# Kernel tuning notes

Measured on AMD Instinct MI355X. Metric: run time of the kernel, lower is better.

Reference implementation:

```python
import jax, jax.numpy as jnp
import numpy as np

WEIGHT_SP = 0.1
BANDWIDTH = 0.5
EPS = 1e-5


def _l2_normalize(v, axis, eps=1e-12):
    # matches torch F.normalize(p=2): x / max(||x||, eps)
    n = jnp.sqrt(jnp.sum(v * v, axis=axis, keepdims=True))
    return v / jnp.maximum(n, eps)


def _compute_meshgrid(N, H, W):
    rows = jnp.arange(H, dtype=jnp.float32) / (H + 1)
    cols = jnp.arange(W, dtype=jnp.float32) / (W + 1)
    gr, gc = jnp.meshgrid(rows, cols, indexing="ij")
    grid = jnp.stack([gr, gc])[None]  # (1, 2, H, W)
    return jnp.broadcast_to(grid, (N, 2, H, W))


def _l2_distance(x, y):
    # Faithful to the torch code; its broadcasting is only valid for N == 1.
    N, C, H, W = x.shape
    xv = x.reshape(N, C, -1)
    yv = y.reshape(N, C, -1)
    x_s = jnp.sum(xv ** 2, axis=1)          # (N, HW)
    y_s = jnp.sum(yv ** 2, axis=1)          # (N, HW)
    A = jnp.einsum("nci,ncj->nij", yv, xv)  # (N, HW, HW)
    dist = y_s - 2.0 * A + x_s.T            # same broadcast as torch (N==1)
    dist = jnp.swapaxes(dist, 1, 2)         # transpose(1,2); reshape is no-op
    return jnp.maximum(dist, 0.0)


def _cosine_distance(x, y):
    y_mu = jnp.mean(y, axis=(0, 2, 3), keepdims=True)   # (1, C, 1, 1)
    xn = _l2_normalize(x - y_mu, axis=1)
    yn = _l2_normalize(y - y_mu, axis=1)
    N, C = x.shape[:2]
    xn = xn.reshape(N, C, -1)
    yn = yn.reshape(N, C, -1)
    cos = jnp.einsum("nci,ncj->nij", xn, yn)            # (N, HW, HW)
    return 1.0 - cos


def _relative_distance(dist, eps=1e-5):
    dmin = jnp.min(dist, axis=2, keepdims=True)
    return dist / (dmin + eps)


def _compute_cx(dist_tilde, bandwidth):
    w = jnp.exp((1.0 - dist_tilde) / bandwidth)
    return w / jnp.sum(w, axis=2, keepdims=True)


def setup_inputs() -> dict:
    key = jax.random.key(0)
    k1, k2 = jax.random.split(key)
    x = jax.random.normal(k1, (1, 512, 80, 80), dtype=jnp.float32)
    y = jax.random.normal(k2, (1, 512, 80, 80), dtype=jnp.float32)
    return {"x": x, "y": y}


def reference(x, y):
    N, C, H, W = x.shape
    # spatial branch
    grid = _compute_meshgrid(N, H, W)
    cx_sp = _compute_cx(_relative_distance(_l2_distance(grid, grid), 1e-5), BANDWIDTH)
    # feature branch (loss_type == 'cosine')
    cx_feat = _compute_cx(_relative_distance(_cosine_distance(x, y), EPS), BANDWIDTH)
    cx_combine = (1.0 - WEIGHT_SP) * cx_feat + WEIGHT_SP * cx_sp
    k_max = jnp.max(cx_combine, axis=2, keepdims=True)  # (N, HW, 1)
    cx = jnp.mean(k_max, axis=1)                        # (N, 1)
    return jnp.mean(-jnp.log(cx + EPS))
```

## Files before the change

### kernel.cpp

```cpp
#include <hip/hip_runtime.h>
#include <hip/hip_bf16.h>
#include <math.h>

#define HW 6400
#define NC 512
#define NH 80
#define NW 80
#define NCH 25
#define NSLOT 50
#define NCYS 4
#define JCH 256
#define TI 128
#define BK 64
#define NT16 400
#define NCG 100

typedef __attribute__((ext_vector_type(8))) short short8;
typedef __attribute__((ext_vector_type(4))) float v4f;

#define MU_OFF    0
#define ACC_OFF   512
#define GMAXP_OFF (ACC_OFF + 64)
#define GDIAG_OFF (GMAXP_OFF + HW*NSLOT)
#define ZP_OFF    (GDIAG_OFF + HW)
#define F32_FLOATS (ZP_OFF + HW*NSLOT)
#define XB_BYTE   ((size_t)(((F32_FLOATS*4) + 255) & ~255))
#define YB_BYTE   (XB_BYTE + (size_t)HW*NC*2)
#define G_BYTE    (YB_BYTE + (size_t)HW*NC*2)
#define G_BYTES   ((size_t)NT16 * NT16 * 256)

typedef __attribute__((address_space(1))) unsigned int uint_g;
typedef __attribute__((address_space(3))) unsigned int uint_l;
__device__ __forceinline__ void gload16(const void* g, void* l) {
    __builtin_amdgcn_global_load_lds((const uint_g*)g, (uint_l*)l, 16, 0, 0);
}

__global__ void k_mu(const float* __restrict__ y, float* __restrict__ mu,
                     float* __restrict__ acczero) {
    if (blockIdx.x == 0 && threadIdx.x < 64) acczero[threadIdx.x] = 0.f;
    int c = blockIdx.x;
    const float4* yc4 = (const float4*)(y + (size_t)c * HW);
    float s = 0.f;
    for (int i = threadIdx.x; i < HW / 4; i += 256) {
        float4 v = yc4[i];
        s += (v.x + v.y) + (v.z + v.w);
    }
    __shared__ float red[256];
    red[threadIdx.x] = s;
    __syncthreads();
    for (int off = 128; off > 0; off >>= 1) {
        if (threadIdx.x < off) red[threadIdx.x] += red[threadIdx.x + off];
        __syncthreads();
    }
    if (threadIdx.x == 0) mu[c] = red[0] * (1.0f / HW);
}

__global__ void k_prep(const float* __restrict__ x, const float* __restrict__ y,
                       const float* __restrict__ mu,
                       unsigned short* __restrict__ xb, unsigned short* __restrict__ yb) {
    __shared__ float smu[NC];
    __shared__ float part[64][17];
    __shared__ float ssinv[64];
    __shared__ float tile[64 * 65];
    const int t = threadIdx.x;
    const int i0 = blockIdx.x * 64;
    const int z = blockIdx.y;
    const float* src = z ? y : x;
    unsigned short* dst = z ? yb : xb;

    for (int c = t; c < NC; c += 256) smu[c] = mu[c];
    __syncthreads();

    const int p0 = (t & 15) * 4;
    const int g  = t >> 4;
    float a0 = 0.f, a1 = 0.f, a2 = 0.f, a3 = 0.f;
    #pragma unroll 2
    for (int ch = 0; ch < 8; ++ch) {
        #pragma unroll
        for (int it = 0; it < 4; ++it) {
            int cl = ch * 64 + it * 16 + g;
            float m = smu[cl];
            float4 v = *(const float4*)(src + (size_t)cl * HW + i0 + p0);
            float d0 = v.x - m, d1 = v.y - m, d2 = v.z - m, d3 = v.w - m;
            a0 = fmaf(d0, d0, a0); a1 = fmaf(d1, d1, a1);
            a2 = fmaf(d2, d2, a2); a3 = fmaf(d3, d3, a3);
        }
    }
    part[p0 + 0][g] = a0; part[p0 + 1][g] = a1;
    part[p0 + 2][g] = a2; part[p0 + 3][g] = a3;
    __syncthreads();
    if (t < 64) {
        float s = 0.f;
        #pragma unroll
        for (int k = 0; k < 16; ++k) s += part[t][k];
        ssinv[t] = 1.0f / fmaxf(sqrtf(s), 1e-12f);
    }
    __syncthreads();

    for (int ch = 0; ch < 8; ++ch) {
        #pragma unroll
        for (int it = 0; it < 4; ++it) {
            int cl = ch * 64 + it * 16 + g;
            float m = smu[cl];
            float4 v = *(const float4*)(src + (size_t)cl * HW + i0 + p0);
            int clo = it * 16 + g;
            tile[(p0 + 0) * 65 + clo] = (v.x - m) * ssinv[p0 + 0];
            tile[(p0 + 1) * 65 + clo] = (v.y - m) * ssinv[p0 + 1];
            tile[(p0 + 2) * 65 + clo] = (v.z - m) * ssinv[p0 + 2];
            tile[(p0 + 3) * 65 + clo] = (v.w - m) * ssinv[p0 + 3];
        }
        __syncthreads();
        #pragma unroll
        for (int it = 0; it < 2; ++it) {
            int il = t >> 2;
            int seg = (t & 3) + it * 4;
            unsigned int pk[4];
            #pragma unroll
            for (int p = 0; p < 4; ++p) {
                float v0 = tile[il * 65 + seg * 8 + p * 2];
                float v1 = tile[il * 65 + seg * 8 + p * 2 + 1];
                __hip_bfloat16 h0 = __float2bfloat16(v0);
                __hip_bfloat16 h1 = __float2bfloat16(v1);
                unsigned short u0 = *reinterpret_cast<unsigned short*>(&h0);
                unsigned short u1 = *reinterpret_cast<unsigned short*>(&h1);
                pk[p] = (unsigned int)u0 | ((unsigned int)u1 << 16);
            }
            uint4 val = make_uint4(pk[0], pk[1], pk[2], pk[3]);
            *(uint4*)&dst[(size_t)(i0 + il) * NC + ch * 64 + seg * 8] = val;
        }
        __syncthreads();
    }
}

__device__ __forceinline__ void rmax_epilogue(float (&rmax)[16], float* gmaxp,
                                              int i0, int wr, int wc, int lr, int lg) {
    #pragma unroll
    for (int u = 0; u < 16; ++u) {
        float v = rmax[u];
        v = fmaxf(v, __shfl_xor(v, 1));
        v = fmaxf(v, __shfl_xor(v, 2));
        v = fmaxf(v, __shfl_xor(v, 4));
        v = fmaxf(v, __shfl_xor(v, 8));
        if (lr == 0) {
            int row = i0 + wr * 64 + (u >> 2) * 16 + lg * 4 + (u & 3);
            gmaxp[(size_t)row * NSLOT + blockIdx.y * 2 + wc] = v;
        }
    }
}

template <typename F>
__device__ __forceinline__ void gemm_driver(const unsigned short* __restrict__ Xb,
                                            const unsigned short* __restrict__ Yb,
                                            F&& consume) {
    __shared__ char sA[TI * BK * 2];
    __shared__ char sB[TI * BK * 2];
    const int t = threadIdx.x;
    const int w = t >> 6, l = t & 63;
    const int wr = w >> 1, wc = w & 1;
    const int lr = l & 15, lg = l >> 4;
    const int i0 = blockIdx.x * TI;
    const int jbase = blockIdx.y * JCH;

    int aoff[4][2], boff[4][2];
    #pragma unroll
    for (int mt = 0; mt < 4; ++mt) {
        int row = wr * 64 + mt * 16 + lr;
        #pragma unroll
        for (int ks = 0; ks < 2; ++ks) {
            int seg = ks * 4 + lg;
            aoff[mt][ks] = row * 128 + ((seg ^ (row & 7)) * 16);
        }
    }
    #pragma unroll
    for (int nt = 0; nt < 4; ++nt) {
        int row = wc * 64 + nt * 16 + lr;
        #pragma unroll
        for (int ks = 0; ks < 2; ++ks) {
            int seg = ks * 4 + lg;
            boff[nt][ks] = row * 128 + ((seg ^ (row & 7)) * 16);
        }
    }
    const int strow = l >> 3;
    const int stcol = ((l & 7) ^ strow) * 8;
    char* dA0 = sA + (w * 4 + 0) * 1024;
    char* dA1 = sA + (w * 4 + 1) * 1024;
    char* dA2 = sA + (w * 4 + 2) * 1024;
    char* dA3 = sA + (w * 4 + 3) * 1024;
    char* dB0 = sB + (w * 4 + 0) * 1024;
    char* dB1 = sB + (w * 4 + 1) * 1024;
    char* dB2 = sB + (w * 4 + 2) * 1024;
    char* dB3 = sB + (w * 4 + 3) * 1024;
    const unsigned short* ga = Xb + (size_t)(i0 + w * 32 + strow) * NC + stcol;
    const unsigned short* gb0 = Yb + (size_t)(jbase + w * 32 + strow) * NC + stcol;

    #pragma unroll 1
    for (int jt = 0; jt < JCH; jt += TI) {
        const unsigned short* gb = gb0 + (size_t)jt * NC;
        v4f acc[4][4];
        #pragma unroll
        for (int mt = 0; mt < 4; ++mt)
            #pragma unroll
            for (int nt = 0; nt < 4; ++nt)
                acc[mt][nt] = (v4f){0.f, 0.f, 0.f, 0.f};

        #pragma unroll 1
        for (int kt = 0; kt < NC; kt += BK) {
            __syncthreads();
            gload16(ga + kt,           dA0);
            gload16(ga + 8  * NC + kt, dA1);
            gload16(ga + 16 * NC + kt, dA2);
            gload16(ga + 24 * NC + kt, dA3);
            gload16(gb + kt,           dB0);
            gload16(gb + 8  * NC + kt, dB1);
            gload16(gb + 16 * NC + kt, dB2);
            gload16(gb + 24 * NC + kt, dB3);
            __syncthreads();
            #pragma unroll
            for (int ks = 0; ks < 2; ++ks) {
                short8 af[4], bf[4];
                #pragma unroll
                for (int mt = 0; mt < 4; ++mt) af[mt] = *(const short8*)&sA[aoff[mt][ks]];
                #pragma unroll
                for (int nt = 0; nt < 4; ++nt) bf[nt] = *(const short8*)&sB[boff[nt][ks]];
                #pragma unroll
                for (int mt = 0; mt < 4; ++mt)
                    #pragma unroll
                    for (int nt = 0; nt < 4; ++nt)
                        acc[mt][nt] = __builtin_amdgcn_mfma_f32_16x16x32_bf16(
                            af[mt], bf[nt], acc[mt][nt], 0, 0, 0);
            }
        }
        consume(acc, jt);
    }
}

__global__ __launch_bounds__(256, 2) void k_pass1s(const unsigned short* __restrict__ Xb,
                                                   const unsigned short* __restrict__ Yb,
                                                   float* __restrict__ gmaxp,
                                                   float* __restrict__ gdiag,
                                                   unsigned int* __restrict__ G1) {
    const int t = threadIdx.x;
    const int w = t >> 6, l = t & 63;
    const int wr = w >> 1, wc = w & 1;
    const int lr = l & 15, lg = l >> 4;
    const int i0 = blockIdx.x * TI;
    const int jbase = blockIdx.y * JCH;
    float rmax[16];
    #pragma unroll
    for (int u = 0; u < 16; ++u) rmax[u] = -3.0e38f;

    gemm_driver(Xb, Yb, [&](v4f (&acc)[4][4], int jt) {
        const bool diagblk = (jbase + jt == i0);
        const int cg = (jbase + jt) / 64 + wc;
        #pragma unroll
        for (int mt = 0; mt < 4; ++mt) {
            unsigned int pks[4];
            #pragma unroll
            for (int nt = 0; nt < 4; ++nt) {
                float g0 = acc[mt][nt][0];
                float g1 = acc[mt][nt][1];
                float g2 = acc[mt][nt][2];
                float g3 = acc[mt][nt][3];
                rmax[mt * 4 + 0] = fmaxf(rmax[mt * 4 + 0], g0);
                rmax[mt * 4 + 1] = fmaxf(rmax[mt * 4 + 1], g1);
                rmax[mt * 4 + 2] = fmaxf(rmax[mt * 4 + 2], g2);
                rmax[mt * 4 + 3] = fmaxf(rmax[mt * 4 + 3], g3);
                unsigned int pk = __builtin_amdgcn_cvt_pk_fp8_f32(g0, g1, 0, false);
                pk = __builtin_amdgcn_cvt_pk_fp8_f32(g2, g3, pk, true);
                pks[nt] = pk;
                if (diagblk) {
                    int rowb = i0 + wr * 64 + mt * 16 + lg * 4;
                    int col = jbase + jt + wc * 64 + nt * 16 + lr;
                    if (col == rowb + 0) gdiag[col] = g0;
                    if (col == rowb + 1) gdiag[col] = g1;
                    if (col == rowb + 2) gdiag[col] = g2;
                    if (col == rowb + 3) gdiag[col] = g3;
                }
            }
            size_t idx = ((size_t)(i0 / 16 + wr * 4 + mt) * NCG + cg) * 64 + l;
            ((uint4*)G1)[idx] = make_uint4(pks[0], pks[1], pks[2], pks[3]);
        }
    });
    rmax_epilogue(rmax, gmaxp, i0, wr, wc, lr, lg);
}

__global__ __launch_bounds__(256) void k_pass2s(const unsigned int* __restrict__ G1,
                                                const float* __restrict__ gmaxp,
                                                float* __restrict__ zp) {
    const int t = threadIdx.x;
    const int w = t >> 6, l = t & 63;
    const int lr = l & 15, lg = l >> 4;
    const int rt = blockIdx.x * 4 + w;
    const int cy = blockIdx.y;

    float m = -3.0e38f;
    {
        int row = rt * 16 + lr;
        #pragma unroll
        for (int k = 0; k < 13; ++k) {
            int s = lg + 4 * k;
            if (s < NSLOT) m = fmaxf(m, gmaxp[(size_t)row * NSLOT + s]);
        }
        m = fmaxf(m, __shfl_xor(m, 16));
        m = fmaxf(m, __shfl_xor(m, 32));
    }
    float inv_lr = 1.0f / ((1.0f - m) + 1e-5f);
    float c1[4], c2[4];
    #pragma unroll
    for (int r = 0; r < 4; ++r) {
        float iv = __shfl(inv_lr, lg * 4 + r);
        c2[r] = 2.0f * iv;
        c1[r] = 2.0f - 2.0f * iv;
    }

    const uint4* base = (const uint4*)G1 + (size_t)rt * (NCG * 64) + l;
    float zs[4] = {0.f, 0.f, 0.f, 0.f};
    #pragma unroll 2
    for (int cgk = cy * 25; cgk < cy * 25 + 25; ++cgk) {
        uint4 v = base[(size_t)cgk * 64];
        #pragma unroll
        for (int q = 0; q < 4; ++q) {
            unsigned int pk = (q == 0) ? v.x : (q == 1) ? v.y : (q == 2) ? v.z : v.w;
            float g0 = __builtin_amdgcn_cvt_f32_fp8(pk, 0);
            float g1 = __builtin_amdgcn_cvt_f32_fp8(pk, 1);
            float g2 = __builtin_amdgcn_cvt_f32_fp8(pk, 2);
            float g3 = __builtin_amdgcn_cvt_f32_fp8(pk, 3);
            zs[0] += __expf(fmaf(c2[0], g0, c1[0]));
            zs[1] += __expf(fmaf(c2[1], g1, c1[1]));
            zs[2] += __expf(fmaf(c2[2], g2, c1[2]));
            zs[3] += __expf(fmaf(c2[3], g3, c1[3]));
        }
    }
    #pragma unroll
    for (int r = 0; r < 4; ++r) {
        float z = zs[r];
        z += __shfl_xor(z, 1);
        z += __shfl_xor(z, 2);
        z += __shfl_xor(z, 4);
        z += __shfl_xor(z, 8);
        if (lr == 0) {
            int row = rt * 16 + lg * 4 + r;
            zp[(size_t)row * NCYS + cy] = z;
        }
    }
}

__global__ void k_kmax_s(const float* __restrict__ zp, const float* __restrict__ gdiag,
                         const float* __restrict__ gmaxp, float* __restrict__ accum,
                         int* __restrict__ counter, float* __restrict__ out) {
    int i = blockIdx.x * 256 + threadIdx.x;
    float Z = 0.f, gmax = -3.0e38f;
    #pragma unroll
    for (int s = 0; s < NCYS; ++s) Z += zp[(size_t)i * NCYS + s];
    #pragma unroll
    for (int s = 0; s < NSLOT; ++s) gmax = fmaxf(gmax, gmaxp[(size_t)i * NSLOT + s]);
    float dmin = 1.0f - gmax;
    float inv = 1.0f / (dmin + 1e-5f);
    float wmx = __expf(2.0f - 2.0f * dmin * inv);
    float wii = __expf(2.0f - 2.0f * (1.0f - gdiag[i]) * inv);
    float invZ = 1.0f / Z;
    float kmax = fmaxf(0.9f * wmx * invZ, 0.9f * wii * invZ + 0.1f);

    __shared__ float red[256];
    red[threadIdx.x] = kmax;
    __syncthreads();
    for (int off = 128; off > 0; off >>= 1) {
        if (threadIdx.x < off) red[threadIdx.x] += red[threadIdx.x + off];
        __syncthreads();
    }
    if (threadIdx.x == 0) {
        atomicAdd(accum, red[0]);
        __threadfence();
        int n = atomicAdd(counter, 1);
        if (n == (int)gridDim.x - 1) {
            float total = atomicAdd(accum, 0.0f);
            out[0] = -logf(total * (1.0f / HW) + 1e-5f);
        }
    }
}

__global__ __launch_bounds__(256, 2) void k_pass1(const unsigned short* __restrict__ Xb,
                                                  const unsigned short* __restrict__ Yb,
                                                  float* __restrict__ gmaxp) {
    const int t = threadIdx.x;
    const int w = t >> 6, l = t & 63;
    const int wr = w >> 1, wc = w & 1;
    const int lr = l & 15, lg = l >> 4;
    const int i0 = blockIdx.x * TI;
    float rmax[16];
    #pragma unroll
    for (int u = 0; u < 16; ++u) rmax[u] = -3.0e38f;
    gemm_driver(Xb, Yb, [&](v4f (&acc)[4][4], int jt) {
        (void)jt;
        #pragma unroll
        for (int mt = 0; mt < 4; ++mt)
            #pragma unroll
            for (int r = 0; r < 4; ++r) {
                float mm = acc[mt][0][r];
                #pragma unroll
                for (int nt = 1; nt < 4; ++nt) mm = fmaxf(mm, acc[mt][nt][r]);
                rmax[mt * 4 + r] = fmaxf(rmax[mt * 4 + r], mm);
            }
    });
    rmax_epilogue(rmax, gmaxp, i0, wr, wc, lr, lg);
}

__global__ void k_invd(const float* __restrict__ gmaxp, float* __restrict__ invd) {
    int i = blockIdx.x * 256 + threadIdx.x;
    float m = -3.0e38f;
    #pragma unroll
    for (int s = 0; s < NSLOT; ++s) m = fmaxf(m, gmaxp[(size_t)i * NSLOT + s]);
    invd[i] = 1.0f / ((1.0f - m) + 1e-5f);
}

__global__ __launch_bounds__(256, 2) void k_pass2(const unsigned short* __restrict__ Xb,
                                                  const unsigned short* __restrict__ Yb,
                                                  const float* __restrict__ invd,
                                                  float* __restrict__ zp) {
    const int t = threadIdx.x;
    const int w = t >> 6, l = t & 63;
    const int wr = w >> 1, wc = w & 1;
    const int lr = l & 15, lg = l >> 4;
    const int i0 = blockIdx.x * TI;
    float zs[16], c1[16], c2[16];
    #pragma unroll
    for (int u = 0; u < 16; ++u) {
        int row = i0 + wr * 64 + (u >> 2) * 16 + lg * 4 + (u & 3);
        float inv = invd[row];
        c2[u] = 2.0f * inv;
        c1[u] = 2.0f - 2.0f * inv;
        zs[u] = 0.f;
    }
    gemm_driver(Xb, Yb, [&](v4f (&acc)[4][4], int jt) {
        (void)jt;
        #pragma unroll
        for (int mt = 0; mt < 4; ++mt)
            #pragma unroll
            for (int r = 0; r < 4; ++r) {
                int u = mt * 4 + r;
                float s = 0.f;
                #pragma unroll
                for (int nt = 0; nt < 4; ++nt)
                    s += __expf(fmaf(c2[u], acc[mt][nt][r], c1[u]));
                zs[u] += s;
            }
    });
    #pragma unroll
    for (int u = 0; u < 16; ++u) {
        float z = zs[u];
        z += __shfl_xor(z, 1);
        z += __shfl_xor(z, 2);
        z += __shfl_xor(z, 4);
        z += __shfl_xor(z, 8);
        if (lr == 0) {
            int row = i0 + wr * 64 + (u >> 2) * 16 + lg * 4 + (u & 3);
            zp[(size_t)row * NSLOT + blockIdx.y * 2 + wc] = z;
        }
    }
}

__global__ void k_kmax(const float* __restrict__ zp, const float* __restrict__ gmaxp,
                       const unsigned short* __restrict__ Xb, const unsigned short* __restrict__ Yb,
                       float* __restrict__ accum, int* __restrict__ counter,
                       float* __restrict__ out) {
    int i = blockIdx.x * 256 + threadIdx.x;
    float Z = 0.f, gmax = -3.0e38f;
    #pragma unroll
    for (int s = 0; s < NSLOT; ++s) {
        Z += zp[(size_t)i * NSLOT + s];
        gmax = fmaxf(gmax, gmaxp[(size_t)i * NSLOT + s]);
    }
    float gii = 0.f;
    const uint2* xr = (const uint2*)(Xb + (size_t)i * NC);
    const uint2* yr = (const uint2*)(Yb + (size_t)i * NC);
    for (int c4 = 0; c4 < NC / 4; ++c4) {
        uint2 xa = xr[c4], ya = yr[c4];
        float x0 = __uint_as_float((xa.x & 0xFFFFu) << 16), y0 = __uint_as_float((ya.x & 0xFFFFu) << 16);
        float x1 = __uint_as_float(xa.x & 0xFFFF0000u),     y1 = __uint_as_float(ya.x & 0xFFFF0000u);
        float x2 = __uint_as_float((xa.y & 0xFFFFu) << 16), y2 = __uint_as_float((ya.y & 0xFFFFu) << 16);
        float x3 = __uint_as_float(xa.y & 0xFFFF0000u),     y3 = __uint_as_float(ya.y & 0xFFFF0000u);
        gii = fmaf(x0, y0, gii); gii = fmaf(x1, y1, gii);
        gii = fmaf(x2, y2, gii); gii = fmaf(x3, y3, gii);
    }
    float dmin = 1.0f - gmax;
    float inv = 1.0f / (dmin + 1e-5f);
    float wmx = __expf(2.0f - 2.0f * dmin * inv);
    float wii = __expf(2.0f - 2.0f * (1.0f - gii) * inv);
    float invZ = 1.0f / Z;
    float kmax = fmaxf(0.9f * wmx * invZ, 0.9f * wii * invZ + 0.1f);

    __shared__ float red[256];
    red[threadIdx.x] = kmax;
    __syncthreads();
    for (int off = 128; off > 0; off >>= 1) {
        if (threadIdx.x < off) red[threadIdx.x] += red[threadIdx.x + off];
        __syncthreads();
    }
    if (threadIdx.x == 0) {
        atomicAdd(accum, red[0]);
        __threadfence();
        int n = atomicAdd(counter, 1);
        if (n == (int)gridDim.x - 1) {
            float total = atomicAdd(accum, 0.0f);
            out[0] = -logf(total * (1.0f / HW) + 1e-5f);
        }
    }
}

extern "C" void kernel_launch(void* const* d_in, const int* in_sizes, int n_in,
                              void* d_out, int out_size, void* d_ws, size_t ws_size,
                              hipStream_t stream) {
    const float* x = (const float*)d_in[0];
    const float* y = (const float*)d_in[1];
    float* out = (float*)d_out;
    float* ws = (float*)d_ws;

    float* mu    = ws + MU_OFF;
    float* accum = ws + ACC_OFF;
    int*   counter = (int*)(accum + 1);
    float* gmaxp = ws + GMAXP_OFF;
    float* gdiag = ws + GDIAG_OFF;
    float* zp    = ws + ZP_OFF;
    unsigned short* Xb = (unsigned short*)((char*)d_ws + XB_BYTE);
    unsigned short* Yb = (unsigned short*)((char*)d_ws + YB_BYTE);
    unsigned int*   G1 = (unsigned int*)((char*)d_ws + G_BYTE);

    const bool bigws = ws_size >= (G_BYTE + G_BYTES);

    hipLaunchKernelGGL(k_mu, dim3(NC), dim3(256), 0, stream, y, mu, accum);
    hipLaunchKernelGGL(k_prep, dim3(HW / 64, 2), dim3(256), 0, stream, x, y, mu, Xb, Yb);

    dim3 grid(HW / TI, NCH);
    if (bigws) {
        hipLaunchKernelGGL(k_pass1s, grid, dim3(256), 0, stream, Xb, Yb, gmaxp, gdiag, G1);
        hipLaunchKernelGGL(k_pass2s, dim3(NT16 / 4, NCYS), dim3(256), 0, stream, G1, gmaxp, zp);
        hipLaunchKernelGGL(k_kmax_s, dim3(HW / 256), dim3(256), 0, stream, zp, gdiag, gmaxp,
                           accum, counter, out);
    } else {
        hipLaunchKernelGGL(k_pass1, grid, dim3(256), 0, stream, Xb, Yb, gmaxp);
        hipLaunchKernelGGL(k_invd, dim3(HW / 256), dim3(256), 0, stream, gmaxp, gdiag);
        hipLaunchKernelGGL(k_pass2, grid, dim3(256), 0, stream, Xb, Yb, gdiag, zp);
        hipLaunchKernelGGL(k_kmax, dim3(HW / 256), dim3(256), 0, stream, zp, gmaxp, Xb, Yb,
                           accum, counter, out);
    }
}
```

Measured before the change: 147.2 us.

## Double-buffer GEMM LDS tiles with prefetch and halve prep tile width

The shared GEMM driver now uses two LDS buffers. It issues the global-to-LDS loads for the next k-step, or the next j-tile, right after the barrier, then runs MFMAs on the current buffer. This drops one barrier per k-step and overlaps memory loads with compute, at the cost of doubling LDS per block, which may limit occupancy. Separately, k_prep handles 32 spatial positions per block instead of 64, doubling its grid for more parallelism.

```diff
diff --git a/kernel.cpp b/kernel.cpp
--- a/kernel.cpp
+++ b/kernel.cpp
@@ -59,11 +59,11 @@
                        const float* __restrict__ mu,
                        unsigned short* __restrict__ xb, unsigned short* __restrict__ yb) {
     __shared__ float smu[NC];
-    __shared__ float part[64][17];
-    __shared__ float ssinv[64];
-    __shared__ float tile[64 * 65];
+    __shared__ float part[32][33];
+    __shared__ float ssinv[32];
+    __shared__ float tile[32 * 65];
     const int t = threadIdx.x;
-    const int i0 = blockIdx.x * 64;
+    const int i0 = blockIdx.x * 32;
     const int z = blockIdx.y;
     const float* src = z ? y : x;
     unsigned short* dst = z ? yb : xb;
@@ -71,49 +71,45 @@
     for (int c = t; c < NC; c += 256) smu[c] = mu[c];
     __syncthreads();
 
-    const int p0 = (t & 15) * 4;
-    const int g  = t >> 4;
+    const int p0 = (t & 7) * 4;
+    const int g  = t >> 3;
     float a0 = 0.f, a1 = 0.f, a2 = 0.f, a3 = 0.f;
-    #pragma unroll 2
-    for (int ch = 0; ch < 8; ++ch) {
-        #pragma unroll
-        for (int it = 0; it < 4; ++it) {
-            int cl = ch * 64 + it * 16 + g;
-            float m = smu[cl];
-            float4 v = *(const float4*)(src + (size_t)cl * HW + i0 + p0);
-            float d0 = v.x - m, d1 = v.y - m, d2 = v.z - m, d3 = v.w - m;
-            a0 = fmaf(d0, d0, a0); a1 = fmaf(d1, d1, a1);
-            a2 = fmaf(d2, d2, a2); a3 = fmaf(d3, d3, a3);
-        }
+    #pragma unroll 4
+    for (int ch = 0; ch < 16; ++ch) {
+        int cl = ch * 32 + g;
+        float m = smu[cl];
+        float4 v = *(const float4*)(src + (size_t)cl * HW + i0 + p0);
+        float d0 = v.x - m, d1 = v.y - m, d2 = v.z - m, d3 = v.w - m;
+        a0 = fmaf(d0, d0, a0); a1 = fmaf(d1, d1, a1);
+        a2 = fmaf(d2, d2, a2); a3 = fmaf(d3, d3, a3);
     }
     part[p0 + 0][g] = a0; part[p0 + 1][g] = a1;
     part[p0 + 2][g] = a2; part[p0 + 3][g] = a3;
     __syncthreads();
-    if (t < 64) {
+    if (t < 32) {
         float s = 0.f;
         #pragma unroll
-        for (int k = 0; k < 16; ++k) s += part[t][k];
+        for (int k = 0; k < 32; ++k) s += part[t][k];
         ssinv[t] = 1.0f / fmaxf(sqrtf(s), 1e-12f);
     }
     __syncthreads();
 
     for (int ch = 0; ch < 8; ++ch) {
         #pragma unroll
-        for (int it = 0; it < 4; ++it) {
-            int cl = ch * 64 + it * 16 + g;
+        for (int it = 0; it < 2; ++it) {
+            int cl = ch * 64 + it * 32 + g;
             float m = smu[cl];
             float4 v = *(const float4*)(src + (size_t)cl * HW + i0 + p0);
-            int clo = it * 16 + g;
+            int clo = it * 32 + g;
             tile[(p0 + 0) * 65 + clo] = (v.x - m) * ssinv[p0 + 0];
             tile[(p0 + 1) * 65 + clo] = (v.y - m) * ssinv[p0 + 1];
             tile[(p0 + 2) * 65 + clo] = (v.z - m) * ssinv[p0 + 2];
             tile[(p0 + 3) * 65 + clo] = (v.w - m) * ssinv[p0 + 3];
         }
         __syncthreads();
-        #pragma unroll
-        for (int it = 0; it < 2; ++it) {
-            int il = t >> 2;
-            int seg = (t & 3) + it * 4;
+        {
+            int il = t >> 3;
+            int seg = t & 7;
             unsigned int pk[4];
             #pragma unroll
             for (int p = 0; p < 4; ++p) {
@@ -152,8 +148,8 @@
 __device__ __forceinline__ void gemm_driver(const unsigned short* __restrict__ Xb,
                                             const unsigned short* __restrict__ Yb,
                                             F&& consume) {
-    __shared__ char sA[TI * BK * 2];
-    __shared__ char sB[TI * BK * 2];
+    __shared__ char sA[2 * TI * BK * 2];
+    __shared__ char sB[2 * TI * BK * 2];
     const int t = threadIdx.x;
     const int w = t >> 6, l = t & 63;
     const int wr = w >> 1, wc = w & 1;
@@ -182,20 +178,29 @@
     }
     const int strow = l >> 3;
     const int stcol = ((l & 7) ^ strow) * 8;
-    char* dA0 = sA + (w * 4 + 0) * 1024;
-    char* dA1 = sA + (w * 4 + 1) * 1024;
-    char* dA2 = sA + (w * 4 + 2) * 1024;
-    char* dA3 = sA + (w * 4 + 3) * 1024;
-    char* dB0 = sB + (w * 4 + 0) * 1024;
-    char* dB1 = sB + (w * 4 + 1) * 1024;
-    char* dB2 = sB + (w * 4 + 2) * 1024;
-    char* dB3 = sB + (w * 4 + 3) * 1024;
     const unsigned short* ga = Xb + (size_t)(i0 + w * 32 + strow) * NC + stcol;
     const unsigned short* gb0 = Yb + (size_t)(jbase + w * 32 + strow) * NC + stcol;
 
+    auto issue = [&](int jt, int kt, int buf) {
+        char* dA = sA + (buf << 14) + w * 4096;
+        char* dB = sB + (buf << 14) + w * 4096;
+        const unsigned short* gaa = ga + kt;
+        const unsigned short* gbb = gb0 + (size_t)jt * NC + kt;
+        gload16(gaa,           dA);
+        gload16(gaa +  8 * NC, dA + 1024);
+        gload16(gaa + 16 * NC, dA + 2048);
+        gload16(gaa + 24 * NC, dA + 3072);
+        gload16(gbb,           dB);
+        gload16(gbb +  8 * NC, dB + 1024);
+        gload16(gbb + 16 * NC, dB + 2048);
+        gload16(gbb + 24 * NC, dB + 3072);
+    };
+
+    int cur = 0;
+    issue(0, 0, 0);
+
     #pragma unroll 1
     for (int jt = 0; jt < JCH; jt += TI) {
-        const unsigned short* gb = gb0 + (size_t)jt * NC;
         v4f acc[4][4];
         #pragma unroll
         for (int mt = 0; mt < 4; ++mt)
@@ -206,22 +211,20 @@
         #pragma unroll 1
         for (int kt = 0; kt < NC; kt += BK) {
             __syncthreads();
-            gload16(ga + kt,           dA0);
-            gload16(ga + 8  * NC + kt, dA1);
-            gload16(ga + 16 * NC + kt, dA2);
-            gload16(ga + 24 * NC + kt, dA3);
-            gload16(gb + kt,           dB0);
-            gload16(gb + 8  * NC + kt, dB1);
-            gload16(gb + 16 * NC + kt, dB2);
-            gload16(gb + 24 * NC + kt, dB3);
-            __syncthreads();
+            {
+                int nkt = kt + BK, njt = jt;
+                if (nkt == NC) { nkt = 0; njt += TI; }
+                if (njt < JCH) issue(njt, nkt, cur ^ 1);
+            }
+            const char* bA = sA + (cur << 14);
+            const char* bB = sB + (cur << 14);
             #pragma unroll
             for (int ks = 0; ks < 2; ++ks) {
                 short8 af[4], bf[4];
                 #pragma unroll
-                for (int mt = 0; mt < 4; ++mt) af[mt] = *(const short8*)&sA[aoff[mt][ks]];
+                for (int mt = 0; mt < 4; ++mt) af[mt] = *(const short8*)&bA[aoff[mt][ks]];
                 #pragma unroll
-                for (int nt = 0; nt < 4; ++nt) bf[nt] = *(const short8*)&sB[boff[nt][ks]];
+                for (int nt = 0; nt < 4; ++nt) bf[nt] = *(const short8*)&bB[boff[nt][ks]];
                 #pragma unroll
                 for (int mt = 0; mt < 4; ++mt)
                     #pragma unroll
@@ -229,6 +232,7 @@
                         acc[mt][nt] = __builtin_amdgcn_mfma_f32_16x16x32_bf16(
                             af[mt], bf[nt], acc[mt][nt], 0, 0, 0);
             }
+            cur ^= 1;
         }
         consume(acc, jt);
     }
@@ -528,7 +532,7 @@
     const bool bigws = ws_size >= (G_BYTE + G_BYTES);
 
     hipLaunchKernelGGL(k_mu, dim3(NC), dim3(256), 0, stream, y, mu, accum);
-    hipLaunchKernelGGL(k_prep, dim3(HW / 64, 2), dim3(256), 0, stream, x, y, mu, Xb, Yb);
+    hipLaunchKernelGGL(k_prep, dim3(HW / 32, 2), dim3(256), 0, stream, x, y, mu, Xb, Yb);
 
     dim3 grid(HW / TI, NCH);
     if (bigws) {
```

New measurement: 160.7 us. 1.09x slower.

## Double pass-1 grid chunks and fuse final kmax reduction into pass-2

Applied to the files above, without the earlier changes.

Halves the column chunk size so the GEMM pass-1 grid has twice as many blocks (more per-row max slots), improving occupancy across CUs. The separate k_kmax_s launch is removed; pass-2 writes the reduced row max, and the last block to finish (via an atomic counter) computes the final reduction and the loss. This saves a kernel launch and the redundant 100-slot max scan, at the cost of a serial tail in one block and more partial-max traffic.

```diff
diff --git a/kernel.cpp b/kernel.cpp
--- a/kernel.cpp
+++ b/kernel.cpp
@@ -6,10 +6,10 @@
 #define NC 512
 #define NH 80
 #define NW 80
-#define NCH 25
-#define NSLOT 50
+#define NCH 50
+#define NSLOT 100
 #define NCYS 4
-#define JCH 256
+#define JCH 128
 #define TI 128
 #define BK 64
 #define NT16 400
@@ -21,7 +21,8 @@
 #define MU_OFF    0
 #define ACC_OFF   512
 #define GMAXP_OFF (ACC_OFF + 64)
-#define GDIAG_OFF (GMAXP_OFF + HW*NSLOT)
+#define GMAXR_OFF (GMAXP_OFF + HW*NSLOT)
+#define GDIAG_OFF (GMAXR_OFF + HW)
 #define ZP_OFF    (GDIAG_OFF + HW)
 #define F32_FLOATS (ZP_OFF + HW*NSLOT)
 #define XB_BYTE   ((size_t)(((F32_FLOATS*4) + 255) & ~255))
@@ -286,7 +287,12 @@
 
 __global__ __launch_bounds__(256) void k_pass2s(const unsigned int* __restrict__ G1,
                                                 const float* __restrict__ gmaxp,
-                                                float* __restrict__ zp) {
+                                                const float* __restrict__ gdiag,
+                                                float* __restrict__ gmaxr,
+                                                float* __restrict__ zp,
+                                                float* __restrict__ accum,
+                                                int* __restrict__ counter,
+                                                float* __restrict__ out) {
     const int t = threadIdx.x;
     const int w = t >> 6, l = t & 63;
     const int lr = l & 15, lg = l >> 4;
@@ -297,13 +303,14 @@
     {
         int row = rt * 16 + lr;
         #pragma unroll
-        for (int k = 0; k < 13; ++k) {
+        for (int k = 0; k < 25; ++k) {
             int s = lg + 4 * k;
-            if (s < NSLOT) m = fmaxf(m, gmaxp[(size_t)row * NSLOT + s]);
+            m = fmaxf(m, gmaxp[(size_t)row * NSLOT + s]);
         }
         m = fmaxf(m, __shfl_xor(m, 16));
         m = fmaxf(m, __shfl_xor(m, 32));
     }
+    if (cy == 0 && lg == 0) gmaxr[rt * 16 + lr] = m;
     float inv_lr = 1.0f / ((1.0f - m) + 1e-5f);
     float c1[4], c2[4];
     #pragma unroll
@@ -343,39 +350,33 @@
             zp[(size_t)row * NCYS + cy] = z;
         }
     }
-}
-
-__global__ void k_kmax_s(const float* __restrict__ zp, const float* __restrict__ gdiag,
-                         const float* __restrict__ gmaxp, float* __restrict__ accum,
-                         int* __restrict__ counter, float* __restrict__ out) {
-    int i = blockIdx.x * 256 + threadIdx.x;
-    float Z = 0.f, gmax = -3.0e38f;
-    #pragma unroll
-    for (int s = 0; s < NCYS; ++s) Z += zp[(size_t)i * NCYS + s];
-    #pragma unroll
-    for (int s = 0; s < NSLOT; ++s) gmax = fmaxf(gmax, gmaxp[(size_t)i * NSLOT + s]);
-    float dmin = 1.0f - gmax;
-    float inv = 1.0f / (dmin + 1e-5f);
-    float wmx = __expf(2.0f - 2.0f * dmin * inv);
-    float wii = __expf(2.0f - 2.0f * (1.0f - gdiag[i]) * inv);
-    float invZ = 1.0f / Z;
-    float kmax = fmaxf(0.9f * wmx * invZ, 0.9f * wii * invZ + 0.1f);
-
-    __shared__ float red[256];
-    red[threadIdx.x] = kmax;
+
+    __shared__ int slast;
+    __threadfence();
+    if (t == 0) slast = atomicAdd(counter, 1);
     __syncthreads();
-    for (int off = 128; off > 0; off >>= 1) {
-        if (threadIdx.x < off) red[threadIdx.x] += red[threadIdx.x + off];
+    if (slast == (int)(gridDim.x * gridDim.y) - 1) {
+        __threadfence();
+        float local = 0.f;
+        for (int i = t; i < HW; i += 256) {
+            float Z = zp[(size_t)i * NCYS + 0] + zp[(size_t)i * NCYS + 1]
+                    + zp[(size_t)i * NCYS + 2] + zp[(size_t)i * NCYS + 3];
+            float gmax = gmaxr[i];
+            float dmin = 1.0f - gmax;
+            float inv = 1.0f / (dmin + 1e-5f);
+            float wmx = __expf(2.0f - 2.0f * dmin * inv);
+            float wii = __expf(2.0f - 2.0f * (1.0f - gdiag[i]) * inv);
+            float invZ = 1.0f / Z;
+            local += fmaxf(0.9f * wmx * invZ, 0.9f * wii * invZ + 0.1f);
+        }
+        __shared__ float red[256];
+        red[t] = local;
         __syncthreads();
-    }
-    if (threadIdx.x == 0) {
-        atomicAdd(accum, red[0]);
-        __threadfence();
-        int n = atomicAdd(counter, 1);
-        if (n == (int)gridDim.x - 1) {
-            float total = atomicAdd(accum, 0.0f);
-            out[0] = -logf(total * (1.0f / HW) + 1e-5f);
-        }
+        for (int off = 128; off > 0; off >>= 1) {
+            if (t < off) red[t] += red[t + off];
+            __syncthreads();
+        }
+        if (t == 0) out[0] = -logf(red[0] * (1.0f / HW) + 1e-5f);
     }
 }
 
@@ -519,6 +520,7 @@
     float* accum = ws + ACC_OFF;
     int*   counter = (int*)(accum + 1);
     float* gmaxp = ws + GMAXP_OFF;
+    float* gmaxr = ws + GMAXR_OFF;
     float* gdiag = ws + GDIAG_OFF;
     float* zp    = ws + ZP_OFF;
     unsigned short* Xb = (unsigned short*)((char*)d_ws + XB_BYTE);
@@ -533,9 +535,8 @@
     dim3 grid(HW / TI, NCH);
     if (bigws) {
         hipLaunchKernelGGL(k_pass1s, grid, dim3(256), 0, stream, Xb, Yb, gmaxp, gdiag, G1);
-        hipLaunchKernelGGL(k_pass2s, dim3(NT16 / 4, NCYS), dim3(256), 0, stream, G1, gmaxp, zp);
-        hipLaunchKernelGGL(k_kmax_s, dim3(HW / 256), dim3(256), 0, stream, zp, gdiag, gmaxp,
-                           accum, counter, out);
+        hipLaunchKernelGGL(k_pass2s, dim3(NT16 / 4, NCYS), dim3(256), 0, stream,
+                           G1, gmaxp, gdiag, gmaxr, zp, accum, counter, out);
     } else {
         hipLaunchKernelGGL(k_pass1, grid, dim3(256), 0, stream, Xb, Yb, gmaxp);
         hipLaunchKernelGGL(k_invd, dim3(HW / 256), dim3(256), 0, stream, gmaxp, gdiag);
```

New measurement: 195.3 us. 1.33x slower.

## Double pass-1 column chunks and precompute row max in a separate kernel

Applied to the files above, without the earlier changes.

Pass 1 now splits the column dimension into 50 chunks of 128 columns instead of 25 of 256, which doubles the grid and the per-row partial-max slots. Pass 2 splits work into 10 column groups instead of 4. A new small kernel reduces the 100 partial maxima per row once, so pass 2 and the final kernel no longer each redo that reduction. This is meant to raise occupancy and parallelism on a large GPU, at the cost of an extra launch, more partial-max traffic and more redundant GEMM prologue work.

```diff
diff --git a/kernel.cpp b/kernel.cpp
--- a/kernel.cpp
+++ b/kernel.cpp
@@ -6,10 +6,10 @@
 #define NC 512
 #define NH 80
 #define NW 80
-#define NCH 25
-#define NSLOT 50
-#define NCYS 4
-#define JCH 256
+#define NCH 50
+#define NSLOT 100
+#define NCYS 10
+#define JCH 128
 #define TI 128
 #define BK 64
 #define NT16 400
@@ -21,7 +21,8 @@
 #define MU_OFF    0
 #define ACC_OFF   512
 #define GMAXP_OFF (ACC_OFF + 64)
-#define GDIAG_OFF (GMAXP_OFF + HW*NSLOT)
+#define GMAXR_OFF (GMAXP_OFF + HW*NSLOT)
+#define GDIAG_OFF (GMAXR_OFF + HW)
 #define ZP_OFF    (GDIAG_OFF + HW)
 #define F32_FLOATS (ZP_OFF + HW*NSLOT)
 #define XB_BYTE   ((size_t)(((F32_FLOATS*4) + 255) & ~255))
@@ -284,8 +285,16 @@
     rmax_epilogue(rmax, gmaxp, i0, wr, wc, lr, lg);
 }
 
+__global__ void k_gmaxr(const float* __restrict__ gmaxp, float* __restrict__ gmaxr) {
+    int i = blockIdx.x * 256 + threadIdx.x;
+    float m = -3.0e38f;
+    #pragma unroll 4
+    for (int s = 0; s < NSLOT; ++s) m = fmaxf(m, gmaxp[(size_t)i * NSLOT + s]);
+    gmaxr[i] = m;
+}
+
 __global__ __launch_bounds__(256) void k_pass2s(const unsigned int* __restrict__ G1,
-                                                const float* __restrict__ gmaxp,
+                                                const float* __restrict__ gmaxr,
                                                 float* __restrict__ zp) {
     const int t = threadIdx.x;
     const int w = t >> 6, l = t & 63;
@@ -293,22 +302,11 @@
     const int rt = blockIdx.x * 4 + w;
     const int cy = blockIdx.y;
 
-    float m = -3.0e38f;
-    {
-        int row = rt * 16 + lr;
-        #pragma unroll
-        for (int k = 0; k < 13; ++k) {
-            int s = lg + 4 * k;
-            if (s < NSLOT) m = fmaxf(m, gmaxp[(size_t)row * NSLOT + s]);
-        }
-        m = fmaxf(m, __shfl_xor(m, 16));
-        m = fmaxf(m, __shfl_xor(m, 32));
-    }
-    float inv_lr = 1.0f / ((1.0f - m) + 1e-5f);
     float c1[4], c2[4];
     #pragma unroll
     for (int r = 0; r < 4; ++r) {
-        float iv = __shfl(inv_lr, lg * 4 + r);
+        float gm = gmaxr[rt * 16 + lg * 4 + r];
+        float iv = 1.0f / ((1.0f - gm) + 1e-5f);
         c2[r] = 2.0f * iv;
         c1[r] = 2.0f - 2.0f * iv;
     }
@@ -316,7 +314,7 @@
     const uint4* base = (const uint4*)G1 + (size_t)rt * (NCG * 64) + l;
     float zs[4] = {0.f, 0.f, 0.f, 0.f};
     #pragma unroll 2
-    for (int cgk = cy * 25; cgk < cy * 25 + 25; ++cgk) {
+    for (int cgk = cy * 10; cgk < cy * 10 + 10; ++cgk) {
         uint4 v = base[(size_t)cgk * 64];
         #pragma unroll
         for (int q = 0; q < 4; ++q) {
@@ -346,14 +344,13 @@
 }
 
 __global__ void k_kmax_s(const float* __restrict__ zp, const float* __restrict__ gdiag,
-                         const float* __restrict__ gmaxp, float* __restrict__ accum,
+                         const float* __restrict__ gmaxr, float* __restrict__ accum,
                          int* __restrict__ counter, float* __restrict__ out) {
     int i = blockIdx.x * 256 + threadIdx.x;
-    float Z = 0.f, gmax = -3.0e38f;
+    float Z = 0.f;
     #pragma unroll
     for (int s = 0; s < NCYS; ++s) Z += zp[(size_t)i * NCYS + s];
-    #pragma unroll
-    for (int s = 0; s < NSLOT; ++s) gmax = fmaxf(gmax, gmaxp[(size_t)i * NSLOT + s]);
+    float gmax = gmaxr[i];
     float dmin = 1.0f - gmax;
     float inv = 1.0f / (dmin + 1e-5f);
     float wmx = __expf(2.0f - 2.0f * dmin * inv);
@@ -408,7 +405,7 @@
 __global__ void k_invd(const float* __restrict__ gmaxp, float* __restrict__ invd) {
     int i = blockIdx.x * 256 + threadIdx.x;
     float m = -3.0e38f;
-    #pragma unroll
+    #pragma unroll 4
     for (int s = 0; s < NSLOT; ++s) m = fmaxf(m, gmaxp[(size_t)i * NSLOT + s]);
     invd[i] = 1.0f / ((1.0f - m) + 1e-5f);
 }
@@ -459,17 +456,14 @@
     }
 }
 
-__global__ void k_kmax(const float* __restrict__ zp, const float* __restrict__ gmaxp,
+__global__ void k_kmax(const float* __restrict__ zp, const float* __restrict__ invd,
                        const unsigned short* __restrict__ Xb, const unsigned short* __restrict__ Yb,
                        float* __restrict__ accum, int* __restrict__ counter,
                        float* __restrict__ out) {
     int i = blockIdx.x * 256 + threadIdx.x;
-    float Z = 0.f, gmax = -3.0e38f;
-    #pragma unroll
-    for (int s = 0; s < NSLOT; ++s) {
-        Z += zp[(size_t)i * NSLOT + s];
-        gmax = fmaxf(gmax, gmaxp[(size_t)i * NSLOT + s]);
-    }
+    float Z = 0.f;
+    #pragma unroll
+    for (int s = 0; s < NSLOT; ++s) Z += zp[(size_t)i * NSLOT + s];
     float gii = 0.f;
     const uint2* xr = (const uint2*)(Xb + (size_t)i * NC);
     const uint2* yr = (const uint2*)(Yb + (size_t)i * NC);
@@ -482,8 +476,8 @@
         gii = fmaf(x0, y0, gii); gii = fmaf(x1, y1, gii);
         gii = fmaf(x2, y2, gii); gii = fmaf(x3, y3, gii);
     }
-    float dmin = 1.0f - gmax;
-    float inv = 1.0f / (dmin + 1e-5f);
+    float inv = invd[i];
+    float dmin = 1.0f / inv - 1e-5f;
     float wmx = __expf(2.0f - 2.0f * dmin * inv);
     float wii = __expf(2.0f - 2.0f * (1.0f - gii) * inv);
     float invZ = 1.0f / Z;
@@ -519,6 +513,7 @@
     float* accum = ws + ACC_OFF;
     int*   counter = (int*)(accum + 1);
     float* gmaxp = ws + GMAXP_OFF;
+    float* gmaxr = ws + GMAXR_OFF;
     float* gdiag = ws + GDIAG_OFF;
     float* zp    = ws + ZP_OFF;
     unsigned short* Xb = (unsigned short*)((char*)d_ws + XB_BYTE);
@@ -533,14 +528,15 @@
     dim3 grid(HW / TI, NCH);
     if (bigws) {
         hipLaunchKernelGGL(k_pass1s, grid, dim3(256), 0, stream, Xb, Yb, gmaxp, gdiag, G1);
-        hipLaunchKernelGGL(k_pass2s, dim3(NT16 / 4, NCYS), dim3(256), 0, stream, G1, gmaxp, zp);
-        hipLaunchKernelGGL(k_kmax_s, dim3(HW / 256), dim3(256), 0, stream, zp, gdiag, gmaxp,
+        hipLaunchKernelGGL(k_gmaxr, dim3(HW / 256), dim3(256), 0, stream, gmaxp, gmaxr);
+        hipLaunchKernelGGL(k_pass2s, dim3(NT16 / 4, NCYS), dim3(256), 0, stream, G1, gmaxr, zp);
+        hipLaunchKernelGGL(k_kmax_s, dim3(HW / 256), dim3(256), 0, stream, zp, gdiag, gmaxr,
                            accum, counter, out);
     } else {
         hipLaunchKernelGGL(k_pass1, grid, dim3(256), 0, stream, Xb, Yb, gmaxp);
         hipLaunchKernelGGL(k_invd, dim3(HW / 256), dim3(256), 0, stream, gmaxp, gdiag);
         hipLaunchKernelGGL(k_pass2, grid, dim3(256), 0, stream, Xb, Yb, gdiag, zp);
-        hipLaunchKernelGGL(k_kmax, dim3(HW / 256), dim3(256), 0, stream, zp, gmaxp, Xb, Yb,
+        hipLaunchKernelGGL(k_kmax, dim3(HW / 256), dim3(256), 0, stream, zp, gdiag, Xb, Yb,
                            accum, counter, out);
     }
 }
```

After: 156.7 us. +6.5%, slower.
